# Kernel optimization log

Measured on AMD Instinct MI355X. Metric: run time of the kernel, lower is better.

The kernel has to match this reference:

```python
import jax, jax.numpy as jnp
import numpy as np

E = 8          # num_experts
TOP_K = 2      # experts per token
D = 1024       # hidden_size
F = 2048       # intermediate_size
B, S = 2, 2048


def setup_inputs() -> dict:
    key = jax.random.key(0)
    k0, k1, k2, k3, k4 = jax.random.split(key, 5)
    return {
        "hidden_states": jax.random.normal(k0, (B, S, D), dtype=jnp.float32),
        "gate_w": jax.random.normal(k1, (D, E), dtype=jnp.float32) * 0.02,
        "w1": jax.random.normal(k2, (E, D, F), dtype=jnp.float32) * 0.02,
        "w2": jax.random.normal(k3, (E, F, D), dtype=jnp.float32) * 0.02,
        "w3": jax.random.normal(k4, (E, D, F), dtype=jnp.float32) * 0.02,
    }


def reference(hidden_states, gate_w, w1, w2, w3):
    b, s, d = hidden_states.shape
    x = hidden_states.reshape(-1, d)                       # [T, D]
    router_logits = x @ gate_w                             # [T, E]
    probs = jax.nn.softmax(router_logits, axis=-1)
    top_w, top_i = jax.lax.top_k(probs, TOP_K)             # [T, K]
    top_w = top_w / jnp.sum(top_w, axis=-1, keepdims=True)

    out = jnp.zeros_like(x)
    for e in range(E):
        # combine weight for expert e per token (0 if not routed here)
        w_e = jnp.sum(jnp.where(top_i == e, top_w, 0.0), axis=-1)   # [T]
        act = jax.nn.silu(x @ w1[e]) * (x @ w3[e])                  # [T, F]
        out = out + (act @ w2[e]) * w_e[:, None]
    return out.reshape(b, s, d)
```

## Files before the change

kernel.cpp:

```cpp
#include <hip/hip_runtime.h>

#define T_TOK 4096
#define D_DIM 1024
#define F_DIM 2048
#define E_NUM 8
#define MAX_TILES 136
#define TZ 16

typedef __attribute__((ext_vector_type(8))) short bf16x8;
typedef __attribute__((ext_vector_type(4))) float f32x4;
typedef unsigned short us;

__device__ __forceinline__ us f2bf(float f) {
  unsigned u = __builtin_bit_cast(unsigned, f);
  unsigned r = 0x7FFFu + ((u >> 16) & 1u);
  return (us)((u + r) >> 16);
}

__device__ __forceinline__ void gload16(const us* g, us* l) {
  __builtin_amdgcn_global_load_lds(
      (const __attribute__((address_space(1))) unsigned int*)g,
      (__attribute__((address_space(3))) unsigned int*)l, 16, 0, 0);
}

__device__ __forceinline__ f32x4 mfma16(bf16x8 a, bf16x8 b, f32x4 c) {
  return __builtin_amdgcn_mfma_f32_16x16x32_bf16(a, b, c, 0, 0, 0);
}

__global__ __launch_bounds__(256) void prep_kernel(
    const float* __restrict__ w1, const float* __restrict__ w3,
    us* __restrict__ W1t, us* __restrict__ W3t,
    const float* __restrict__ x, const float* __restrict__ gw,
    int* __restrict__ route_e, float2* __restrict__ route_w,
    us* __restrict__ Xb) {
  int z = blockIdx.z;
  int tid = threadIdx.x;

  if (z < 16) {
    __shared__ float tile[64][65];
    int which = z >> 3, e = z & 7;
    const float* src = (which == 0 ? w1 : w3);
    us* dst = (which == 0 ? W1t : W3t);
    src += (size_t)e * D_DIM * F_DIM; dst += (size_t)e * D_DIM * F_DIM;
    int bid = blockIdx.y * gridDim.x + blockIdx.x;
    int nbx = F_DIM / 64;
    int i0 = (bid / nbx) * 64, j0 = (bid % nbx) * 64;
    int lr = tid >> 4, lc = (tid & 15) * 4;
    #pragma unroll
    for (int p = 0; p < 4; p++) {
      int row = p * 16 + lr;
      float4 v = *(const float4*)&src[(size_t)(i0 + row) * F_DIM + j0 + lc];
      tile[row][lc + 0] = v.x; tile[row][lc + 1] = v.y;
      tile[row][lc + 2] = v.z; tile[row][lc + 3] = v.w;
    }
    __syncthreads();
    #pragma unroll
    for (int p = 0; p < 4; p++) {
      int orow = p * 16 + lr;
      us b0 = f2bf(tile[lc + 0][orow]);
      us b1 = f2bf(tile[lc + 1][orow]);
      us b2 = f2bf(tile[lc + 2][orow]);
      us b3 = f2bf(tile[lc + 3][orow]);
      uint2 o;
      o.x = b0 | ((unsigned)b1 << 16);
      o.y = b2 | ((unsigned)b3 << 16);
      *(uint2*)&dst[(size_t)(j0 + orow) * D_DIM + i0 + lc] = o;
    }
  } else {
    int bid = (z - 16) * 512 + blockIdx.y * gridDim.x + blockIdx.x;
    int lane = tid & 63;
    int t = bid * 4 + (tid >> 6);
    float acc[E_NUM];
    #pragma unroll
    for (int e = 0; e < E_NUM; e++) acc[e] = 0.f;
    const float* xr = x + (size_t)t * D_DIM;
    us* xbr = Xb + (size_t)t * D_DIM;
    #pragma unroll
    for (int j = 0; j < D_DIM / 64; j++) {
      int d = lane + 64 * j;
      float xv = xr[d];
      xbr[d] = f2bf(xv);
      const float4* g = reinterpret_cast<const float4*>(gw + (size_t)d * E_NUM);
      float4 g0 = g[0], g1 = g[1];
      acc[0] += xv * g0.x; acc[1] += xv * g0.y; acc[2] += xv * g0.z; acc[3] += xv * g0.w;
      acc[4] += xv * g1.x; acc[5] += xv * g1.y; acc[6] += xv * g1.z; acc[7] += xv * g1.w;
    }
    #pragma unroll
    for (int e = 0; e < E_NUM; e++) {
      #pragma unroll
      for (int off = 32; off > 0; off >>= 1) acc[e] += __shfl_xor(acc[e], off);
    }
    if (lane == 0) {
      int e1 = 0; float l1 = acc[0];
      #pragma unroll
      for (int e = 1; e < E_NUM; e++) { if (acc[e] > l1) { l1 = acc[e]; e1 = e; } }
      int e2 = -1; float l2 = -1e30f;
      #pragma unroll
      for (int e = 0; e < E_NUM; e++) { if (e != e1 && acc[e] > l2) { l2 = acc[e]; e2 = e; } }
      float wa = 1.f / (1.f + expf(l2 - l1));
      float wb = 1.f / (1.f + expf(l1 - l2));
      route_e[t] = e1 | (e2 << 8);
      route_w[t] = make_float2(wa, wb);
    }
  }
}

__global__ __launch_bounds__(1024) void scatter_kernel(
    const int* __restrict__ route_e, const float2* __restrict__ route_w,
    int* __restrict__ counts, int4* __restrict__ tiles,
    int* __restrict__ list, float* __restrict__ wts) {
  int tid = threadIdx.x;
  int lane = tid & 63, wv = tid >> 6;
  __shared__ int wave_tot[16][E_NUM];
  __shared__ int wave_base[16][E_NUM];
  __shared__ int tot_s[E_NUM];

  int e_loc[8]; float w_loc[8];
  #pragma unroll
  for (int j = 0; j < 4; j++) {
    int t = tid * 4 + j;
    int re = route_e[t];
    float2 rw = route_w[t];
    e_loc[2 * j]     = re & 0xff; w_loc[2 * j]     = rw.x;
    e_loc[2 * j + 1] = re >> 8;   w_loc[2 * j + 1] = rw.y;
  }
  int c[E_NUM], pre[E_NUM];
  #pragma unroll
  for (int e = 0; e < E_NUM; e++) {
    int s = 0;
    #pragma unroll
    for (int j = 0; j < 8; j++) s += (e_loc[j] == e) ? 1 : 0;
    c[e] = s;
  }
  #pragma unroll
  for (int e = 0; e < E_NUM; e++) {
    int v = c[e];
    #pragma unroll
    for (int off = 1; off < 64; off <<= 1) {
      int u = __shfl_up(v, off);
      if (lane >= off) v += u;
    }
    pre[e] = v - c[e];
    if (lane == 63) wave_tot[wv][e] = v;
  }
  __syncthreads();
  if (tid < E_NUM) {
    int s = 0;
    for (int w = 0; w < 16; w++) { wave_base[w][tid] = s; s += wave_tot[w][tid]; }
    tot_s[tid] = s;
    counts[tid] = s;
  }
  __syncthreads();
  #pragma unroll
  for (int j = 0; j < 8; j++) {
    int e = e_loc[j];
    int off = 0;
    #pragma unroll
    for (int jj = 0; jj < 8; jj++)
      if (jj < j) off += (e_loc[jj] == e) ? 1 : 0;
    int basee = 0, pree = 0;
    #pragma unroll
    for (int ee = 0; ee < E_NUM; ee++)
      if (e == ee) { basee = wave_base[wv][ee]; pree = pre[ee]; }
    int pos = basee + pree + off;
    int t = tid * 4 + (j >> 1);
    list[e * T_TOK + pos] = t * 2 + (j & 1);
    wts[e * T_TOK + pos]  = w_loc[j];
  }
  if (tid < MAX_TILES) {
    int4 tt; tt.x = -1; tt.y = 0; tt.z = 0; tt.w = 0;
    int s = 0;
    #pragma unroll
    for (int e = 0; e < E_NUM; e++) {
      int ntl = (tot_s[e] + 63) >> 6;
      if (tid >= s && tid < s + ntl) { tt.x = e; tt.y = (tid - s) * 64; tt.z = tot_s[e]; }
      s += ntl;
    }
    tiles[tid] = tt;
  }
}

__global__ __launch_bounds__(256, 4) void gemm1_kernel(
    const us* __restrict__ Xb,
    const us* __restrict__ W1t,
    const us* __restrict__ W3t,
    const int4* __restrict__ tiles, const int* __restrict__ list,
    us* __restrict__ H,
    const float* __restrict__ w2, us* __restrict__ W2t) {
  __shared__ __align__(16) us smem[3 * 64 * 64];
  __shared__ int rid_s[64];
  int tid = threadIdx.x;

  if (blockIdx.y < TZ) {
    float (*tile)[65] = (float(*)[65])smem;
    int slot = blockIdx.y * 32 + blockIdx.x;
    int i0 = (slot >> 4) * 64;
    int j0 = (slot & 15) * 64;
    int lr = tid >> 4, lc = (tid & 15) * 4;
    #pragma unroll 1
    for (int e = 0; e < E_NUM; e++) {
      const float* src = w2 + (size_t)e * F_DIM * D_DIM;
      us* dst = W2t + (size_t)e * F_DIM * D_DIM;
      #pragma unroll
      for (int p = 0; p < 4; p++) {
        int row = p * 16 + lr;
        float4 v = *(const float4*)&src[(size_t)(i0 + row) * D_DIM + j0 + lc];
        tile[row][lc + 0] = v.x; tile[row][lc + 1] = v.y;
        tile[row][lc + 2] = v.z; tile[row][lc + 3] = v.w;
      }
      __syncthreads();
      #pragma unroll
      for (int p = 0; p < 4; p++) {
        int orow = p * 16 + lr;
        us b0 = f2bf(tile[lc + 0][orow]);
        us b1 = f2bf(tile[lc + 1][orow]);
        us b2 = f2bf(tile[lc + 2][orow]);
        us b3 = f2bf(tile[lc + 3][orow]);
        uint2 o;
        o.x = b0 | ((unsigned)b1 << 16);
        o.y = b2 | ((unsigned)b3 << 16);
        *(uint2*)&dst[(size_t)(j0 + orow) * F_DIM + i0 + lc] = o;
      }
      __syncthreads();
    }
    return;
  }

  us* As  = smem;
  us* B1s = smem + 4096;
  us* B3s = smem + 8192;

  int4 td = tiles[blockIdx.y - TZ];
  int e = td.x;
  if (e < 0) return;
  int base = td.y, cnt = td.z;
  int nt = blockIdx.x;

  if (tid < 64) {
    int r = base + tid; if (r > cnt - 1) r = cnt - 1;
    rid_s[tid] = list[e * T_TOK + r];
  }
  __syncthreads();

  int lane = tid & 63, wid = tid >> 6;
  int sr = lane >> 3;
  int sg = (lane & 7) ^ sr;
  const us* a_src[2];
  #pragma unroll
  for (int t = 0; t < 2; t++)
    a_src[t] = Xb + (size_t)(rid_s[wid * 16 + t * 8 + sr] >> 1) * D_DIM + sg * 8;
  const us *b1_src[2], *b3_src[2];
  #pragma unroll
  for (int t = 0; t < 2; t++) {
    size_t row = (size_t)e * F_DIM + nt * 64 + wid * 16 + t * 8 + sr;
    b1_src[t] = W1t + row * D_DIM + sg * 8;
    b3_src[t] = W3t + row * D_DIM + sg * 8;
  }

  int wm = (wid >> 1) * 32, wn = (wid & 1) * 32;
  int frow = lane & 15;
  int fk = lane >> 4;

  unsigned offA[2][2], offB[2][2];
  #pragma unroll
  for (int mf = 0; mf < 2; mf++)
    #pragma unroll
    for (int kc = 0; kc < 2; kc++) {
      int m = wm + mf * 16 + frow, gk = kc * 4 + fk;
      offA[mf][kc] = m * 64 + ((gk ^ (m & 7)) * 8);
    }
  #pragma unroll
  for (int nf = 0; nf < 2; nf++)
    #pragma unroll
    for (int kc = 0; kc < 2; kc++) {
      int n = wn + nf * 16 + frow, gk = kc * 4 + fk;
      offB[nf][kc] = n * 64 + ((gk ^ (n & 7)) * 8);
    }

  f32x4 acc1[2][2], acc3[2][2];
  #pragma unroll
  for (int mf = 0; mf < 2; mf++)
    #pragma unroll
    for (int nf = 0; nf < 2; nf++) {
      f32x4 z = {0.f, 0.f, 0.f, 0.f};
      acc1[mf][nf] = z; acc3[mf][nf] = z;
    }

  #pragma unroll 1
  for (int k0 = 0; k0 < D_DIM; k0 += 64) {
    #pragma unroll
    for (int t = 0; t < 2; t++) {
      gload16(a_src[t] + k0, &As[(wid * 16 + t * 8) * 64]);
      gload16(b1_src[t] + k0, &B1s[(wid * 16 + t * 8) * 64]);
      gload16(b3_src[t] + k0, &B3s[(wid * 16 + t * 8) * 64]);
    }
    __syncthreads();
    #pragma unroll
    for (int kc = 0; kc < 2; kc++) {
      bf16x8 a[2], b1[2], b3[2];
      #pragma unroll
      for (int mf = 0; mf < 2; mf++) a[mf] = *(const bf16x8*)&As[offA[mf][kc]];
      #pragma unroll
      for (int nf = 0; nf < 2; nf++) {
        b1[nf] = *(const bf16x8*)&B1s[offB[nf][kc]];
        b3[nf] = *(const bf16x8*)&B3s[offB[nf][kc]];
      }
      #pragma unroll
      for (int mf = 0; mf < 2; mf++)
        #pragma unroll
        for (int nf = 0; nf < 2; nf++) {
          acc1[mf][nf] = mfma16(a[mf], b1[nf], acc1[mf][nf]);
          acc3[mf][nf] = mfma16(a[mf], b3[nf], acc3[mf][nf]);
        }
    }
    __syncthreads();
  }

  #pragma unroll
  for (int mf = 0; mf < 2; mf++) {
    #pragma unroll
    for (int i = 0; i < 4; i++) {
      int m = wm + mf * 16 + fk * 4 + i;
      if (base + m < cnt) {
        int rid = rid_s[m];
        us* hrow = H + (size_t)rid * F_DIM + nt * 64 + wn;
        #pragma unroll
        for (int nf = 0; nf < 2; nf++) {
          float z = acc1[mf][nf][i];
          float u = acc3[mf][nf][i];
          hrow[nf * 16 + frow] = f2bf((z / (1.f + expf(-z))) * u);
        }
      }
    }
  }
}

__global__ __launch_bounds__(256, 4) void gemm2_kernel(
    const us* __restrict__ H,
    const us* __restrict__ W2t,
    const int4* __restrict__ tiles, const int* __restrict__ list,
    const float* __restrict__ wts,
    float* __restrict__ out) {
  __shared__ us As[64 * 64];
  __shared__ us Bs[128 * 64];
  __shared__ int rid_s[64];
  __shared__ float wt_s[64];

  int4 td = tiles[blockIdx.y];
  int e = td.x;
  if (e < 0) return;
  int base = td.y, cnt = td.z;
  int nt = blockIdx.x;
  int tid = threadIdx.x;

  if (tid < 64) {
    int r = base + tid; if (r > cnt - 1) r = cnt - 1;
    rid_s[tid] = list[e * T_TOK + r];
    wt_s[tid] = wts[e * T_TOK + r];
  }
  __syncthreads();

  int lane = tid & 63, wid = tid >> 6;
  int sr = lane >> 3;
  int sg = (lane & 7) ^ sr;
  const us* a_src[2];
  #pragma unroll
  for (int t = 0; t < 2; t++)
    a_src[t] = H + (size_t)rid_s[wid * 16 + t * 8 + sr] * F_DIM + sg * 8;
  const us* b_src[4];
  #pragma unroll
  for (int t = 0; t < 4; t++)
    b_src[t] = W2t + ((size_t)e * D_DIM + nt * 128 + wid * 32 + t * 8 + sr) * F_DIM + sg * 8;

  int wm = (wid >> 1) * 32, wn = (wid & 1) * 64;
  int frow = lane & 15;
  int fk = lane >> 4;

  unsigned offA[2][2], offB[4][2];
  #pragma unroll
  for (int mf = 0; mf < 2; mf++)
    #pragma unroll
    for (int kc = 0; kc < 2; kc++) {
      int m = wm + mf * 16 + frow, gk = kc * 4 + fk;
      offA[mf][kc] = m * 64 + ((gk ^ (m & 7)) * 8);
    }
  #pragma unroll
  for (int nf = 0; nf < 4; nf++)
    #pragma unroll
    for (int kc = 0; kc < 2; kc++) {
      int n = wn + nf * 16 + frow, gk = kc * 4 + fk;
      offB[nf][kc] = n * 64 + ((gk ^ (n & 7)) * 8);
    }

  f32x4 acc[2][4];
  #pragma unroll
  for (int mf = 0; mf < 2; mf++)
    #pragma unroll
    for (int nf = 0; nf < 4; nf++) {
      f32x4 z = {0.f, 0.f, 0.f, 0.f};
      acc[mf][nf] = z;
    }

  #pragma unroll 1
  for (int k0 = 0; k0 < F_DIM; k0 += 64) {
    #pragma unroll
    for (int t = 0; t < 2; t++)
      gload16(a_src[t] + k0, &As[(wid * 16 + t * 8) * 64]);
    #pragma unroll
    for (int t = 0; t < 4; t++)
      gload16(b_src[t] + k0, &Bs[(wid * 32 + t * 8) * 64]);
    __syncthreads();
    #pragma unroll
    for (int kc = 0; kc < 2; kc++) {
      bf16x8 a[2], b[4];
      #pragma unroll
      for (int mf = 0; mf < 2; mf++) a[mf] = *(const bf16x8*)&As[offA[mf][kc]];
      #pragma unroll
      for (int nf = 0; nf < 4; nf++) b[nf] = *(const bf16x8*)&Bs[offB[nf][kc]];
      #pragma unroll
      for (int mf = 0; mf < 2; mf++)
        #pragma unroll
        for (int nf = 0; nf < 4; nf++)
          acc[mf][nf] = mfma16(a[mf], b[nf], acc[mf][nf]);
    }
    __syncthreads();
  }

  #pragma unroll
  for (int mf = 0; mf < 2; mf++) {
    #pragma unroll
    for (int i = 0; i < 4; i++) {
      int m = wm + mf * 16 + fk * 4 + i;
      if (base + m < cnt) {
        int tok = rid_s[m] >> 1;
        float w = wt_s[m];
        float* orow = out + (size_t)tok * D_DIM + nt * 128 + wn;
        #pragma unroll
        for (int nf = 0; nf < 4; nf++)
          atomicAdd(&orow[nf * 16 + frow], acc[mf][nf][i] * w);
      }
    }
  }
}

extern "C" void kernel_launch(void* const* d_in, const int* in_sizes, int n_in,
                              void* d_out, int out_size, void* d_ws, size_t ws_size,
                              hipStream_t stream) {
  const float* x  = (const float*)d_in[0];
  const float* gw = (const float*)d_in[1];
  const float* w1 = (const float*)d_in[2];
  const float* w2 = (const float*)d_in[3];
  const float* w3 = (const float*)d_in[4];
  float* out = (float*)d_out;

  char* ws = (char*)d_ws;
  const size_t LISTB = (size_t)E_NUM * T_TOK * 4;
  size_t o_counts  = 0;
  size_t o_tiles   = 256;
  size_t o_route_e = 4096;
  size_t o_route_w = o_route_e + (size_t)T_TOK * 4;
  size_t o_list    = o_route_w + (size_t)T_TOK * 8;
  size_t o_wts     = o_list + LISTB;
  size_t o_Xb      = o_wts + LISTB;
  size_t o_W1t     = o_Xb + (size_t)T_TOK * D_DIM * 2;
  size_t wt_sz     = (size_t)E_NUM * F_DIM * D_DIM * 2;
  size_t o_W3t     = o_W1t + wt_sz;
  size_t o_W2t     = o_W3t + wt_sz;
  size_t o_H       = o_W2t + wt_sz;

  int* counts    = (int*)(ws + o_counts);
  int4* tiles    = (int4*)(ws + o_tiles);
  int* route_e   = (int*)(ws + o_route_e);
  float2* route_w = (float2*)(ws + o_route_w);
  int* list      = (int*)(ws + o_list);
  float* wts     = (float*)(ws + o_wts);
  us* Xb  = (us*)(ws + o_Xb);
  us* W1t = (us*)(ws + o_W1t);
  us* W3t = (us*)(ws + o_W3t);
  us* W2t = (us*)(ws + o_W2t);
  us* H   = (us*)(ws + o_H);

  hipMemsetAsync(out, 0, (size_t)out_size * 4, stream);

  prep_kernel<<<dim3(32, 16, 18), 256, 0, stream>>>(
      w1, w3, W1t, W3t, x, gw, route_e, route_w, Xb);

  scatter_kernel<<<dim3(1), 1024, 0, stream>>>(route_e, route_w, counts,
                                               tiles, list, wts);

  gemm1_kernel<<<dim3(F_DIM / 64, TZ + MAX_TILES), 256, 0, stream>>>(
      Xb, W1t, W3t, tiles, list, H, w2, W2t);
  gemm2_kernel<<<dim3(D_DIM / 128, MAX_TILES), 256, 0, stream>>>(
      H, W2t, tiles, list, wts, out);
}
```

Measured before the change: 233.1 us.

## Load A operand fragments directly from global into registers, bypassing LDS

Both grouped GEMM kernels now fetch the gathered token rows (X for gemm1, H for gemm2) straight from global memory into MFMA fragment registers instead of staging them through shared memory. This drops the A tile from LDS, which cuts LDS traffic and footprint and may allow higher occupancy. The cost is that each wave now reads its own A rows from global with no reuse across waves sharing the same M rows (the two N-waves read duplicate data). These loads are also synchronous register loads issued inside the loop without prefetch, so their latency may be exposed.

```diff
diff --git a/kernel.cpp b/kernel.cpp
--- a/kernel.cpp
+++ b/kernel.cpp
@@ -187,7 +187,7 @@
     const int4* __restrict__ tiles, const int* __restrict__ list,
     us* __restrict__ H,
     const float* __restrict__ w2, us* __restrict__ W2t) {
-  __shared__ __align__(16) us smem[3 * 64 * 64];
+  __shared__ __align__(16) us smem[64 * 65 * 2];
   __shared__ int rid_s[64];
   int tid = threadIdx.x;
 
@@ -226,9 +226,8 @@
     return;
   }
 
-  us* As  = smem;
-  us* B1s = smem + 4096;
-  us* B3s = smem + 8192;
+  us* B1s = smem;
+  us* B3s = smem + 4096;
 
   int4 td = tiles[blockIdx.y - TZ];
   int e = td.x;
@@ -245,10 +244,6 @@
   int lane = tid & 63, wid = tid >> 6;
   int sr = lane >> 3;
   int sg = (lane & 7) ^ sr;
-  const us* a_src[2];
-  #pragma unroll
-  for (int t = 0; t < 2; t++)
-    a_src[t] = Xb + (size_t)(rid_s[wid * 16 + t * 8 + sr] >> 1) * D_DIM + sg * 8;
   const us *b1_src[2], *b3_src[2];
   #pragma unroll
   for (int t = 0; t < 2; t++) {
@@ -261,14 +256,16 @@
   int frow = lane & 15;
   int fk = lane >> 4;
 
-  unsigned offA[2][2], offB[2][2];
-  #pragma unroll
-  for (int mf = 0; mf < 2; mf++)
-    #pragma unroll
-    for (int kc = 0; kc < 2; kc++) {
-      int m = wm + mf * 16 + frow, gk = kc * 4 + fk;
-      offA[mf][kc] = m * 64 + ((gk ^ (m & 7)) * 8);
-    }
+  const us* a_ptr[2][2];
+  #pragma unroll
+  for (int mf = 0; mf < 2; mf++) {
+    int rid = rid_s[wm + mf * 16 + frow] >> 1;
+    #pragma unroll
+    for (int kc = 0; kc < 2; kc++)
+      a_ptr[mf][kc] = Xb + (size_t)rid * D_DIM + (kc * 4 + fk) * 8;
+  }
+
+  unsigned offB[2][2];
   #pragma unroll
   for (int nf = 0; nf < 2; nf++)
     #pragma unroll
@@ -288,18 +285,21 @@
 
   #pragma unroll 1
   for (int k0 = 0; k0 < D_DIM; k0 += 64) {
+    bf16x8 a[2][2];
+    #pragma unroll
+    for (int mf = 0; mf < 2; mf++)
+      #pragma unroll
+      for (int kc = 0; kc < 2; kc++)
+        a[mf][kc] = *(const bf16x8*)(a_ptr[mf][kc] + k0);
     #pragma unroll
     for (int t = 0; t < 2; t++) {
-      gload16(a_src[t] + k0, &As[(wid * 16 + t * 8) * 64]);
       gload16(b1_src[t] + k0, &B1s[(wid * 16 + t * 8) * 64]);
       gload16(b3_src[t] + k0, &B3s[(wid * 16 + t * 8) * 64]);
     }
     __syncthreads();
     #pragma unroll
     for (int kc = 0; kc < 2; kc++) {
-      bf16x8 a[2], b1[2], b3[2];
-      #pragma unroll
-      for (int mf = 0; mf < 2; mf++) a[mf] = *(const bf16x8*)&As[offA[mf][kc]];
+      bf16x8 b1[2], b3[2];
       #pragma unroll
       for (int nf = 0; nf < 2; nf++) {
         b1[nf] = *(const bf16x8*)&B1s[offB[nf][kc]];
@@ -309,8 +309,8 @@
       for (int mf = 0; mf < 2; mf++)
         #pragma unroll
         for (int nf = 0; nf < 2; nf++) {
-          acc1[mf][nf] = mfma16(a[mf], b1[nf], acc1[mf][nf]);
-          acc3[mf][nf] = mfma16(a[mf], b3[nf], acc3[mf][nf]);
+          acc1[mf][nf] = mfma16(a[mf][kc], b1[nf], acc1[mf][nf]);
+          acc3[mf][nf] = mfma16(a[mf][kc], b3[nf], acc3[mf][nf]);
         }
     }
     __syncthreads();
@@ -341,7 +341,6 @@
     const int4* __restrict__ tiles, const int* __restrict__ list,
     const float* __restrict__ wts,
     float* __restrict__ out) {
-  __shared__ us As[64 * 64];
   __shared__ us Bs[128 * 64];
   __shared__ int rid_s[64];
   __shared__ float wt_s[64];
@@ -363,10 +362,6 @@
   int lane = tid & 63, wid = tid >> 6;
   int sr = lane >> 3;
   int sg = (lane & 7) ^ sr;
-  const us* a_src[2];
-  #pragma unroll
-  for (int t = 0; t < 2; t++)
-    a_src[t] = H + (size_t)rid_s[wid * 16 + t * 8 + sr] * F_DIM + sg * 8;
   const us* b_src[4];
   #pragma unroll
   for (int t = 0; t < 4; t++)
@@ -376,14 +371,16 @@
   int frow = lane & 15;
   int fk = lane >> 4;
 
-  unsigned offA[2][2], offB[4][2];
-  #pragma unroll
-  for (int mf = 0; mf < 2; mf++)
-    #pragma unroll
-    for (int kc = 0; kc < 2; kc++) {
-      int m = wm + mf * 16 + frow, gk = kc * 4 + fk;
-      offA[mf][kc] = m * 64 + ((gk ^ (m & 7)) * 8);
-    }
+  const us* a_ptr[2][2];
+  #pragma unroll
+  for (int mf = 0; mf < 2; mf++) {
+    int rid = rid_s[wm + mf * 16 + frow];
+    #pragma unroll
+    for (int kc = 0; kc < 2; kc++)
+      a_ptr[mf][kc] = H + (size_t)rid * F_DIM + (kc * 4 + fk) * 8;
+  }
+
+  unsigned offB[4][2];
   #pragma unroll
   for (int nf = 0; nf < 4; nf++)
     #pragma unroll
@@ -403,25 +400,26 @@
 
   #pragma unroll 1
   for (int k0 = 0; k0 < F_DIM; k0 += 64) {
-    #pragma unroll
-    for (int t = 0; t < 2; t++)
-      gload16(a_src[t] + k0, &As[(wid * 16 + t * 8) * 64]);
+    bf16x8 a[2][2];
+    #pragma unroll
+    for (int mf = 0; mf < 2; mf++)
+      #pragma unroll
+      for (int kc = 0; kc < 2; kc++)
+        a[mf][kc] = *(const bf16x8*)(a_ptr[mf][kc] + k0);
     #pragma unroll
     for (int t = 0; t < 4; t++)
       gload16(b_src[t] + k0, &Bs[(wid * 32 + t * 8) * 64]);
     __syncthreads();
     #pragma unroll
     for (int kc = 0; kc < 2; kc++) {
-      bf16x8 a[2], b[4];
-      #pragma unroll
-      for (int mf = 0; mf < 2; mf++) a[mf] = *(const bf16x8*)&As[offA[mf][kc]];
+      bf16x8 b[4];
       #pragma unroll
       for (int nf = 0; nf < 4; nf++) b[nf] = *(const bf16x8*)&Bs[offB[nf][kc]];
       #pragma unroll
       for (int mf = 0; mf < 2; mf++)
         #pragma unroll
         for (int nf = 0; nf < 4; nf++)
-          acc[mf][nf] = mfma16(a[mf], b[nf], acc[mf][nf]);
+          acc[mf][nf] = mfma16(a[mf][kc], b[nf], acc[mf][nf]);
     }
     __syncthreads();
   }
```

New measurement: 342.4 us. 46.9% more time.
